# Kernel tuning notes

Measured on AMD Instinct MI355X. Metric: run time of the kernel, lower is better.

The kernel has to match this reference:

```python
import jax, jax.numpy as jnp
import numpy as np

INPUT_DIM = 2048
N_EXPERTS = 64
K = 2


def setup_inputs() -> dict:
    key = jax.random.key(0)
    kx, kw, kb = jax.random.split(key, 3)
    x = jax.random.normal(kx, (4, 4096, INPUT_DIM), dtype=jnp.float32)
    # nn.Linear(input_dim, n_experts): weight [n_experts, input_dim], bias [n_experts]
    bound = 1.0 / np.sqrt(INPUT_DIM)
    W = jax.random.uniform(kw, (N_EXPERTS, INPUT_DIM), minval=-bound, maxval=bound, dtype=jnp.float32)
    b = jax.random.uniform(kb, (N_EXPERTS,), minval=-bound, maxval=bound, dtype=jnp.float32)
    return {"x": x, "W": W, "b": b}


def reference(x, W, b):
    # logits: [B, S, E]
    logits = jnp.einsum('bsd,ed->bse', x, W) + b
    topk_vals, topk_indices = jax.lax.top_k(logits, K)  # over last (expert) axis
    gate_probs = jax.nn.softmax(topk_vals, axis=-1)
    return gate_probs, topk_indices
```

## Files before the change

### kernel.cpp

```cpp
#include <hip/hip_runtime.h>
#include <math.h>

typedef _Float16 half8 __attribute__((ext_vector_type(8)));
typedef float floatx4 __attribute__((ext_vector_type(4)));

#define NTOK 16384
#define DIM  2048
#define NEXP 64
#define MB   32
#define NBLK (NTOK / MB)
#define WSW_HALF8 (64 * 4 * 64)
#define WSW_BYTES (2 * WSW_HALF8 * 16)

__global__ void wprep_kernel(const float* __restrict__ W, _Float16* __restrict__ wsw) {
    const int id   = blockIdx.x * blockDim.x + threadIdx.x;
    const int lane = id & 63;
    const int tg   = (id >> 6) & 3;
    const int sg   = id >> 8;
    const int e    = tg * 16 + (lane & 15);
    const int k    = sg * 32 + (lane >> 4) * 8;
    const float* src = W + (size_t)e * DIM + k;
    half8 h, l;
#pragma unroll
    for (int j = 0; j < 8; j++) {
        const float v  = src[j];
        const _Float16 hh = (_Float16)v;
        h[j] = hh;
        l[j] = (_Float16)((v - (float)hh) * 2048.0f);
    }
    const size_t slot = (size_t)(sg * 4 + tg) * 64 + lane;
    ((half8*)wsw)[slot]             = h;
    ((half8*)wsw)[WSW_HALF8 + slot] = l;
}

template <bool USE_WS>
__global__ __launch_bounds__(512, 4)
void gating_mfma_kernel(const float* __restrict__ x, const float* __restrict__ W,
                        const _Float16* __restrict__ wsw, const float* __restrict__ bias,
                        float* __restrict__ out)
{
    __shared__ float part[2 * MB * 65];

    const int tid  = threadIdx.x;
    const int lane = tid & 63;
    const int w    = tid >> 6;
    const int mt   = w & 1;
    const int nh   = (w >> 1) & 1;
    const int kh   = w >> 2;
    const int col  = lane & 15;
    const int quad = lane >> 4;
    const int tok0 = blockIdx.x * MB;

    const float* xrow = x + (size_t)(tok0 + mt * 16 + col) * DIM + kh * 1024 + quad * 8;

    floatx4 a0m = {0,0,0,0}, a0l = {0,0,0,0};
    floatx4 a1m = {0,0,0,0}, a1l = {0,0,0,0};

    const half8* bhp = ((const half8*)wsw) + ((size_t)(kh * 32) * 4 + nh * 2) * 64 + lane;
    const half8* blp = bhp + WSW_HALF8;

#pragma unroll 2
    for (int s = 0; s < 32; ++s) {
        const float4 v0 = *(const float4*)(xrow + s * 32);
        const float4 v1 = *(const float4*)(xrow + s * 32 + 4);
        const float av[8] = {v0.x, v0.y, v0.z, v0.w, v1.x, v1.y, v1.z, v1.w};
        half8 ah, al;
#pragma unroll
        for (int j = 0; j < 8; j++) {
            const _Float16 hh = (_Float16)av[j];
            ah[j] = hh;
            al[j] = (_Float16)((av[j] - (float)hh) * 2048.0f);
        }
        half8 bh0, bh1, bl0, bl1;
        if constexpr (USE_WS) {
            bh0 = bhp[s * 256];        bh1 = bhp[s * 256 + 64];
            bl0 = blp[s * 256];        bl1 = blp[s * 256 + 64];
        } else {
            const int k = kh * 1024 + s * 32 + quad * 8;
#pragma unroll
            for (int t = 0; t < 2; t++) {
                const float* wr = W + (size_t)((nh * 2 + t) * 16 + col) * DIM + k;
                const float4 w0 = *(const float4*)(wr);
                const float4 w1 = *(const float4*)(wr + 4);
                const float wv[8] = {w0.x, w0.y, w0.z, w0.w, w1.x, w1.y, w1.z, w1.w};
                half8 h, l;
#pragma unroll
                for (int j = 0; j < 8; j++) {
                    const _Float16 hh = (_Float16)wv[j];
                    h[j] = hh;
                    l[j] = (_Float16)((wv[j] - (float)hh) * 2048.0f);
                }
                if (t == 0) { bh0 = h; bl0 = l; } else { bh1 = h; bl1 = l; }
            }
        }
        a0m = __builtin_amdgcn_mfma_f32_16x16x32_f16(ah, bh0, a0m, 0, 0, 0);
        a1m = __builtin_amdgcn_mfma_f32_16x16x32_f16(ah, bh1, a1m, 0, 0, 0);
        a0l = __builtin_amdgcn_mfma_f32_16x16x32_f16(ah, bl0, a0l, 0, 0, 0);
        a1l = __builtin_amdgcn_mfma_f32_16x16x32_f16(ah, bl1, a1l, 0, 0, 0);
        a0l = __builtin_amdgcn_mfma_f32_16x16x32_f16(al, bh0, a0l, 0, 0, 0);
        a1l = __builtin_amdgcn_mfma_f32_16x16x32_f16(al, bh1, a1l, 0, 0, 0);
    }

    const float inv = 1.0f / 2048.0f;
#pragma unroll
    for (int r = 0; r < 4; r++) {
        const int m = mt * 16 + quad * 4 + r;
        part[(kh * MB + m) * 65 + nh * 32 + col]      = a0m[r] + a0l[r] * inv;
        part[(kh * MB + m) * 65 + nh * 32 + 16 + col] = a1m[r] + a1l[r] * inv;
    }
    __syncthreads();

    if (tid < MB) {
        const int t = tid;
        float v0 = -INFINITY, v1 = -INFINITY;
        int   i0 = 0, i1 = 0;
        for (int e = 0; e < NEXP; e++) {
            const float v = part[t * 65 + e] + part[(MB + t) * 65 + e] + bias[e];
            if (v > v0) { v1 = v0; i1 = i0; v0 = v; i0 = e; }
            else if (v > v1) { v1 = v; i1 = e; }
        }
        const float e1 = expf(v1 - v0);
        const float s  = 1.f + e1;
        const int   g  = tok0 + t;
        out[2 * g + 0] = 1.f / s;
        out[2 * g + 1] = e1 / s;
        out[2 * NTOK + 2 * g + 0] = (float)i0;
        out[2 * NTOK + 2 * g + 1] = (float)i1;
    }
}

extern "C" void kernel_launch(void* const* d_in, const int* in_sizes, int n_in,
                              void* d_out, int out_size, void* d_ws, size_t ws_size,
                              hipStream_t stream) {
    const float* x    = (const float*)d_in[0];
    const float* W    = (const float*)d_in[1];
    const float* bias = (const float*)d_in[2];
    float*       out  = (float*)d_out;
    _Float16*    wsw  = (_Float16*)d_ws;

    if (ws_size >= (size_t)WSW_BYTES) {
        hipLaunchKernelGGL(wprep_kernel, dim3(64), dim3(256), 0, stream, (const float*)d_in[1], wsw);
        hipLaunchKernelGGL((gating_mfma_kernel<true>), dim3(NBLK), dim3(512), 0, stream,
                           x, W, wsw, bias, out);
    } else {
        hipLaunchKernelGGL((gating_mfma_kernel<false>), dim3(NBLK), dim3(512), 0, stream,
                           x, W, wsw, bias, out);
    }
}
```

Before: 226.3 us.

## Retile gating GEMM to 16-token blocks with 4-way K split and register double-buffering

Changes the work split so each wave covers all 64 experts for 16 tokens over a quarter of K, instead of 2 warps per M tile with N and K halved. Block size drops to 256 threads, the LDS partial buffer grows to four K-slices, and the x and weight fragments are prefetched one or two steps ahead in registers, with the loop fully unrolled. This aims to reuse each x fragment across four expert tiles and to hide global load latency, at the cost of more registers per thread and a four-way reduction in the epilogue.

```diff
diff --git a/kernel.cpp b/kernel.cpp
--- a/kernel.cpp
+++ b/kernel.cpp
@@ -4,11 +4,12 @@
 typedef _Float16 half8 __attribute__((ext_vector_type(8)));
 typedef float floatx4 __attribute__((ext_vector_type(4)));
 
-#define NTOK 16384
-#define DIM  2048
-#define NEXP 64
-#define MB   32
-#define NBLK (NTOK / MB)
+#define NTOK  16384
+#define DIM   2048
+#define NEXP  64
+#define MB    16
+#define NBLK  (NTOK / MB)
+#define NSTEP 16
 #define WSW_HALF8 (64 * 4 * 64)
 #define WSW_BYTES (2 * WSW_HALF8 * 16)
 
@@ -33,80 +34,100 @@
     ((half8*)wsw)[WSW_HALF8 + slot] = l;
 }
 
+__device__ __forceinline__ void split_a(const float4& v0, const float4& v1,
+                                        half8& hi, half8& lo) {
+    const float av[8] = {v0.x, v0.y, v0.z, v0.w, v1.x, v1.y, v1.z, v1.w};
+#pragma unroll
+    for (int j = 0; j < 8; j++) {
+        const _Float16 hh = (_Float16)av[j];
+        hi[j] = hh;
+        lo[j] = (_Float16)((av[j] - (float)hh) * 2048.0f);
+    }
+}
+
 template <bool USE_WS>
-__global__ __launch_bounds__(512, 4)
+__global__ __launch_bounds__(256, 4)
 void gating_mfma_kernel(const float* __restrict__ x, const float* __restrict__ W,
                         const _Float16* __restrict__ wsw, const float* __restrict__ bias,
                         float* __restrict__ out)
 {
-    __shared__ float part[2 * MB * 65];
+    __shared__ float part[4 * MB * 65];
 
     const int tid  = threadIdx.x;
     const int lane = tid & 63;
-    const int w    = tid >> 6;
-    const int mt   = w & 1;
-    const int nh   = (w >> 1) & 1;
-    const int kh   = w >> 2;
+    const int kh   = tid >> 6;
     const int col  = lane & 15;
     const int quad = lane >> 4;
     const int tok0 = blockIdx.x * MB;
 
-    const float* xrow = x + (size_t)(tok0 + mt * 16 + col) * DIM + kh * 1024 + quad * 8;
+    const float* xrow = x + (size_t)(tok0 + col) * DIM + kh * 512 + quad * 8;
+    const half8* bh_base = (const half8*)wsw + (size_t)kh * 4096 + lane;
+    const half8* bl_base = bh_base + WSW_HALF8;
 
-    floatx4 a0m = {0,0,0,0}, a0l = {0,0,0,0};
-    floatx4 a1m = {0,0,0,0}, a1l = {0,0,0,0};
+    floatx4 accm[4] = {{0,0,0,0},{0,0,0,0},{0,0,0,0},{0,0,0,0}};
+    floatx4 accl[4] = {{0,0,0,0},{0,0,0,0},{0,0,0,0},{0,0,0,0}};
 
-    const half8* bhp = ((const half8*)wsw) + ((size_t)(kh * 32) * 4 + nh * 2) * 64 + lane;
-    const half8* blp = bhp + WSW_HALF8;
+    float4 xf[2][2];
+    half8  bhf[2][4], blf[2][4];
 
-#pragma unroll 2
-    for (int s = 0; s < 32; ++s) {
-        const float4 v0 = *(const float4*)(xrow + s * 32);
-        const float4 v1 = *(const float4*)(xrow + s * 32 + 4);
-        const float av[8] = {v0.x, v0.y, v0.z, v0.w, v1.x, v1.y, v1.z, v1.w};
-        half8 ah, al;
+    xf[0][0] = *(const float4*)(xrow);
+    xf[0][1] = *(const float4*)(xrow + 4);
+    xf[1][0] = *(const float4*)(xrow + 32);
+    xf[1][1] = *(const float4*)(xrow + 36);
+    if constexpr (USE_WS) {
 #pragma unroll
-        for (int j = 0; j < 8; j++) {
-            const _Float16 hh = (_Float16)av[j];
-            ah[j] = hh;
-            al[j] = (_Float16)((av[j] - (float)hh) * 2048.0f);
+        for (int tg = 0; tg < 4; tg++) { bhf[0][tg] = bh_base[tg * 64]; blf[0][tg] = bl_base[tg * 64]; }
+    } else {
+#pragma unroll
+        for (int tg = 0; tg < 4; tg++) {
+            const float* wr = W + (size_t)(tg * 16 + col) * DIM + kh * 512 + quad * 8;
+            split_a(*(const float4*)(wr), *(const float4*)(wr + 4), bhf[0][tg], blf[0][tg]);
         }
-        half8 bh0, bh1, bl0, bl1;
-        if constexpr (USE_WS) {
-            bh0 = bhp[s * 256];        bh1 = bhp[s * 256 + 64];
-            bl0 = blp[s * 256];        bl1 = blp[s * 256 + 64];
-        } else {
-            const int k = kh * 1024 + s * 32 + quad * 8;
+    }
+
 #pragma unroll
-            for (int t = 0; t < 2; t++) {
-                const float* wr = W + (size_t)((nh * 2 + t) * 16 + col) * DIM + k;
-                const float4 w0 = *(const float4*)(wr);
-                const float4 w1 = *(const float4*)(wr + 4);
-                const float wv[8] = {w0.x, w0.y, w0.z, w0.w, w1.x, w1.y, w1.z, w1.w};
-                half8 h, l;
+    for (int s = 0; s < NSTEP; ++s) {
+        const int cur = s & 1, nxt = cur ^ 1;
+
+        half8 ah, alo;
+        split_a(xf[cur][0], xf[cur][1], ah, alo);
+
+        if (s + 2 < NSTEP) {
+            xf[cur][0] = *(const float4*)(xrow + (s + 2) * 32);
+            xf[cur][1] = *(const float4*)(xrow + (s + 2) * 32 + 4);
+        }
+        if (s + 1 < NSTEP) {
+            if constexpr (USE_WS) {
 #pragma unroll
-                for (int j = 0; j < 8; j++) {
-                    const _Float16 hh = (_Float16)wv[j];
-                    h[j] = hh;
-                    l[j] = (_Float16)((wv[j] - (float)hh) * 2048.0f);
+                for (int tg = 0; tg < 4; tg++) {
+                    bhf[nxt][tg] = bh_base[(s + 1) * 256 + tg * 64];
+                    blf[nxt][tg] = bl_base[(s + 1) * 256 + tg * 64];
                 }
-                if (t == 0) { bh0 = h; bl0 = l; } else { bh1 = h; bl1 = l; }
+            } else {
+#pragma unroll
+                for (int tg = 0; tg < 4; tg++) {
+                    const float* wr = W + (size_t)(tg * 16 + col) * DIM + kh * 512 + (s + 1) * 32 + quad * 8;
+                    split_a(*(const float4*)(wr), *(const float4*)(wr + 4), bhf[nxt][tg], blf[nxt][tg]);
+                }
             }
         }
-        a0m = __builtin_amdgcn_mfma_f32_16x16x32_f16(ah, bh0, a0m, 0, 0, 0);
-        a1m = __builtin_amdgcn_mfma_f32_16x16x32_f16(ah, bh1, a1m, 0, 0, 0);
-        a0l = __builtin_amdgcn_mfma_f32_16x16x32_f16(ah, bl0, a0l, 0, 0, 0);
-        a1l = __builtin_amdgcn_mfma_f32_16x16x32_f16(ah, bl1, a1l, 0, 0, 0);
-        a0l = __builtin_amdgcn_mfma_f32_16x16x32_f16(al, bh0, a0l, 0, 0, 0);
-        a1l = __builtin_amdgcn_mfma_f32_16x16x32_f16(al, bh1, a1l, 0, 0, 0);
+
+#pragma unroll
+        for (int tg = 0; tg < 4; tg++) {
+            accm[tg] = __builtin_amdgcn_mfma_f32_16x16x32_f16(ah,  bhf[cur][tg], accm[tg], 0, 0, 0);
+            accl[tg] = __builtin_amdgcn_mfma_f32_16x16x32_f16(ah,  blf[cur][tg], accl[tg], 0, 0, 0);
+            accl[tg] = __builtin_amdgcn_mfma_f32_16x16x32_f16(alo, bhf[cur][tg], accl[tg], 0, 0, 0);
+        }
     }
 
     const float inv = 1.0f / 2048.0f;
 #pragma unroll
-    for (int r = 0; r < 4; r++) {
-        const int m = mt * 16 + quad * 4 + r;
-        part[(kh * MB + m) * 65 + nh * 32 + col]      = a0m[r] + a0l[r] * inv;
-        part[(kh * MB + m) * 65 + nh * 32 + 16 + col] = a1m[r] + a1l[r] * inv;
+    for (int tg = 0; tg < 4; tg++) {
+#pragma unroll
+        for (int r = 0; r < 4; r++) {
+            const int m = quad * 4 + r;
+            part[(kh * MB + m) * 65 + tg * 16 + col] = accm[tg][r] + accl[tg][r] * inv;
+        }
     }
     __syncthreads();
 
@@ -115,15 +136,17 @@
         float v0 = -INFINITY, v1 = -INFINITY;
         int   i0 = 0, i1 = 0;
         for (int e = 0; e < NEXP; e++) {
-            const float v = part[t * 65 + e] + part[(MB + t) * 65 + e] + bias[e];
+            const float v = part[t * 65 + e] + part[(MB + t) * 65 + e]
+                          + part[(2 * MB + t) * 65 + e] + part[(3 * MB + t) * 65 + e]
+                          + bias[e];
             if (v > v0) { v1 = v0; i1 = i0; v0 = v; i0 = e; }
             else if (v > v1) { v1 = v; i1 = e; }
         }
         const float e1 = expf(v1 - v0);
-        const float s  = 1.f + e1;
+        const float sden = 1.f + e1;
         const int   g  = tok0 + t;
-        out[2 * g + 0] = 1.f / s;
-        out[2 * g + 1] = e1 / s;
+        out[2 * g + 0] = 1.f / sden;
+        out[2 * g + 1] = e1 / sden;
         out[2 * NTOK + 2 * g + 0] = (float)i0;
         out[2 * NTOK + 2 * g + 1] = (float)i1;
     }
@@ -140,10 +163,10 @@
 
     if (ws_size >= (size_t)WSW_BYTES) {
         hipLaunchKernelGGL(wprep_kernel, dim3(64), dim3(256), 0, stream, (const float*)d_in[1], wsw);
-        hipLaunchKernelGGL((gating_mfma_kernel<true>), dim3(NBLK), dim3(512), 0, stream,
+        hipLaunchKernelGGL((gating_mfma_kernel<true>), dim3(NBLK), dim3(256), 0, stream,
                            x, W, wsw, bias, out);
     } else {
-        hipLaunchKernelGGL((gating_mfma_kernel<false>), dim3(NBLK), dim3(512), 0, stream,
+        hipLaunchKernelGGL((gating_mfma_kernel<false>), dim3(NBLK), dim3(256), 0, stream,
                            x, W, wsw, bias, out);
     }
 }
```

Result: faster. 219.9 us (-2.8%).
